# Optimization experiments

Measured on AMD Instinct MI355X. Metric: run time of the kernel, lower is better.

## Reference

```python
import jax, jax.numpy as jnp
import numpy as np

D_MODEL = 1024
H = 16
D_H = D_MODEL // H


def setup_inputs() -> dict:
    key = jax.random.key(0)
    ks = jax.random.split(key, 10)
    B, T_dec, T_enc = 2, 2048, 2048
    s = 1.0 / np.sqrt(D_MODEL)
    return {
        "tgt": jax.random.normal(ks[0], (B, T_dec, D_MODEL), jnp.float32),
        "memory": jax.random.normal(ks[1], (B, T_enc, D_MODEL), jnp.float32),
        "W_q": jax.random.normal(ks[2], (D_MODEL, D_MODEL), jnp.float32) * s,
        "b_q": jnp.zeros((D_MODEL,), jnp.float32),
        "W_k": jax.random.normal(ks[3], (D_MODEL, D_MODEL), jnp.float32) * s,
        "b_k": jnp.zeros((D_MODEL,), jnp.float32),
        "W_v": jax.random.normal(ks[4], (D_MODEL, D_MODEL), jnp.float32) * s,
        "b_v": jnp.zeros((D_MODEL,), jnp.float32),
        "W_o": jax.random.normal(ks[5], (D_MODEL, D_MODEL), jnp.float32) * s,
        "b_o": jnp.zeros((D_MODEL,), jnp.float32),
    }


def reference(tgt, memory, W_q, b_q, W_k, b_k, W_v, b_v, W_o, b_o):
    B, T_dec, _ = tgt.shape
    T_enc = memory.shape[1]
    # Projections (nn.Linear: x @ W^T + b; here W stored as (in,out) so x @ W + b)
    Q = tgt @ W_q + b_q          # (B, T_dec, d_model)
    K = memory @ W_k + b_k       # (B, T_enc, d_model)
    V = memory @ W_v + b_v       # (B, T_enc, d_model)
    # split heads: (B, h, T, d_h)
    Q = Q.reshape(B, T_dec, H, D_H).transpose(0, 2, 1, 3)
    K = K.reshape(B, T_enc, H, D_H).transpose(0, 2, 1, 3)
    V = V.reshape(B, T_enc, H, D_H).transpose(0, 2, 1, 3)
    # scores (B, h, T_dec, T_enc)
    S = jnp.einsum("bhqd,bhkd->bhqk", Q, K) / jnp.sqrt(jnp.float32(D_H)).astype(Q.dtype)
    A = jax.nn.softmax(S, axis=-1)
    Y = jnp.einsum("bhqk,bhkd->bhqd", A, V)
    Y = Y.transpose(0, 2, 1, 3).reshape(B, T_dec, D_MODEL)
    return Y @ W_o + b_o
```

## Files before the change

kernel.cpp:

```cpp
#include <hip/hip_runtime.h>
#include <hip/hip_bf16.h>
#include <stdint.h>

typedef unsigned short u16;
typedef __attribute__((ext_vector_type(8))) short bf16x8;
typedef __attribute__((ext_vector_type(4))) short bf16x4;
typedef __attribute__((ext_vector_type(4))) float f32x4;

__device__ __forceinline__ float bf2f(u16 u) {
    union { unsigned int i; float f; } v; v.i = ((unsigned int)u) << 16; return v.f;
}
__device__ __forceinline__ u16 f2bf(float f) {
    union { float f; unsigned int i; } v; v.f = f;
    unsigned int x = v.i;
    return (u16)((x + 0x7fffu + ((x >> 16) & 1u)) >> 16);
}
__device__ __forceinline__ unsigned fbits(float f) {
    union { float f; unsigned int i; } v; v.f = f; return v.i;
}
__device__ __forceinline__ void async16(const void* g, void* lds) {
    __builtin_amdgcn_global_load_lds((const __attribute__((address_space(1))) void*)g,
                                     (__attribute__((address_space(3))) void*)lds,
                                     16, 0, 0);
}

#define QSCALE 0.18033688f

__global__ __launch_bounds__(256) void prep(
    const float* __restrict__ tgt, const float* __restrict__ mem,
    const float* __restrict__ Wq, const float* __restrict__ Wk,
    const float* __restrict__ Wv, const float* __restrict__ Wo,
    u16* __restrict__ Wt, u16* __restrict__ tgtb, u16* __restrict__ memb)
{
    __shared__ u16 tile[64][65];
    const int id = blockIdx.x;
    const int tid = threadIdx.x;
    if (id < 1024) {
        const int z = id >> 8;
        const float* in = (z == 0) ? Wq : (z == 1) ? Wk : (z == 2) ? Wv : Wo;
        u16* out = Wt + (size_t)z * 1048576;
        const int k0 = (id & 15) * 64, n0 = ((id >> 4) & 15) * 64;
        const int r = tid >> 2, c0 = (tid & 3) << 4;
#pragma unroll
        for (int i = 0; i < 4; ++i) {
            float4 v = *(const float4*)&in[(size_t)(k0 + r) * 1024 + n0 + c0 + i * 4];
            tile[c0 + i * 4 + 0][r] = f2bf(v.x);
            tile[c0 + i * 4 + 1][r] = f2bf(v.y);
            tile[c0 + i * 4 + 2][r] = f2bf(v.z);
            tile[c0 + i * 4 + 3][r] = f2bf(v.w);
        }
        __syncthreads();
#pragma unroll
        for (int i = 0; i < 2; ++i) {
            bf16x8 v;
#pragma unroll
            for (int j = 0; j < 8; ++j) v[j] = (short)tile[r][c0 + i * 8 + j];
            *(bf16x8*)&out[(size_t)(n0 + r) * 1024 + k0 + c0 + i * 8] = v;
        }
    } else {
        size_t i = ((size_t)(id - 1024) * 256 + tid) * 8;
        float4 a0 = *(const float4*)&tgt[i];
        float4 a1 = *(const float4*)&tgt[i + 4];
        float4 b0 = *(const float4*)&mem[i];
        float4 b1 = *(const float4*)&mem[i + 4];
        bf16x8 va, vb;
        va[0] = (short)f2bf(a0.x); va[1] = (short)f2bf(a0.y);
        va[2] = (short)f2bf(a0.z); va[3] = (short)f2bf(a0.w);
        va[4] = (short)f2bf(a1.x); va[5] = (short)f2bf(a1.y);
        va[6] = (short)f2bf(a1.z); va[7] = (short)f2bf(a1.w);
        vb[0] = (short)f2bf(b0.x); vb[1] = (short)f2bf(b0.y);
        vb[2] = (short)f2bf(b0.z); vb[3] = (short)f2bf(b0.w);
        vb[4] = (short)f2bf(b1.x); vb[5] = (short)f2bf(b1.y);
        vb[6] = (short)f2bf(b1.z); vb[7] = (short)f2bf(b1.w);
        *(bf16x8*)&tgtb[i] = va;
        *(bf16x8*)&memb[i] = vb;
    }
}

__global__ __launch_bounds__(256) void gemm_qkv(
    const u16* __restrict__ tgtb, const u16* __restrict__ memb,
    const u16* __restrict__ Wt,
    const float* __restrict__ bq, const float* __restrict__ bk, const float* __restrict__ bv,
    u16* __restrict__ Qb, u16* __restrict__ Kb, u16* __restrict__ Vtb)
{
    __shared__ __align__(16) u16 sA[2][128 * 32];
    __shared__ __align__(16) u16 sB[2][128 * 32];
    const int z = blockIdx.z;
    const u16* A = (z == 0) ? tgtb : memb;
    const u16* Bt = Wt + (size_t)z * 1048576;
    const float* bias = (z == 0) ? bq : (z == 1) ? bk : bv;

    const int tid = threadIdx.x;
    const int wave = tid >> 6, lane = tid & 63;
    const int quad = lane >> 4, l16 = lane & 15;
    const int m0 = blockIdx.x * 128, n0 = blockIdx.y * 128;
    const int wm = (wave & 1) * 64, wn = (wave >> 1) * 64;
    const int sw = (quad ^ ((l16 >> 1) & 3)) << 3;

    f32x4 acc[4][4] = {};

#define GSTAGE(k0, buf)                                                       \
    {                                                                         \
        _Pragma("unroll")                                                     \
        for (int r = 0; r < 2; ++r) {                                         \
            int c = tid + r * 256;                                            \
            int g = (c & 3) ^ ((c >> 3) & 3);                                 \
            const u16* gA = A + (size_t)(m0 + (c >> 2)) * 1024 + (k0) + g * 8;\
            async16(gA, (char*)&sA[buf][0] + r * 4096 + wave * 1024);         \
            const u16* gB = Bt + (size_t)(n0 + (c >> 2)) * 1024 + (k0) + g * 8;\
            async16(gB, (char*)&sB[buf][0] + r * 4096 + wave * 1024);         \
        }                                                                     \
    }

    GSTAGE(0, 0);

    for (int it = 0; it < 32; ++it) {
        __syncthreads();
        if (it < 31) GSTAGE((it + 1) * 32, (it + 1) & 1);
        const u16* a = &sA[it & 1][0];
        const u16* bb_ = &sB[it & 1][0];
        bf16x8 af[4], bfr[4];
#pragma unroll
        for (int i = 0; i < 4; ++i) {
            af[i]  = *(const bf16x8*)&a[(wm + i * 16 + l16) * 32 + sw];
            bfr[i] = *(const bf16x8*)&bb_[(wn + i * 16 + l16) * 32 + sw];
        }
#pragma unroll
        for (int i = 0; i < 4; ++i)
#pragma unroll
            for (int j = 0; j < 4; ++j)
                acc[i][j] = __builtin_amdgcn_mfma_f32_16x16x32_bf16(af[i], bfr[j], acc[i][j], 0, 0, 0);
    }
#undef GSTAGE

    if (z == 2) {
#pragma unroll
        for (int j = 0; j < 4; ++j) {
            int n = n0 + wn + j * 16 + l16;
            float bb = bias[n];
            int d = n & 63;
#pragma unroll
            for (int i = 0; i < 4; ++i) {
                int mb = m0 + wm + i * 16 + quad * 4;
                int bh = (mb >> 11) * 16 + (n >> 6);
                bf16x4 pk;
#pragma unroll
                for (int r = 0; r < 4; ++r) pk[r] = (short)f2bf(acc[i][j][r] + bb);
                *(bf16x4*)&Vtb[(size_t)bh * 131072 + (size_t)d * 2048 + (mb & 2047)] = pk;
            }
        }
    } else {
        u16* C = (z == 0) ? Qb : Kb;
        const float scl = (z == 0) ? QSCALE : 1.0f;
#pragma unroll
        for (int j = 0; j < 4; ++j) {
            int n = n0 + wn + j * 16 + l16;
            float bb = bias[n];
#pragma unroll
            for (int i = 0; i < 4; ++i) {
                int mb = m0 + wm + i * 16 + quad * 4;
#pragma unroll
                for (int r = 0; r < 4; ++r)
                    C[(size_t)(mb + r) * 1024 + n] = f2bf((acc[i][j][r] + bb) * scl);
            }
        }
    }
}

__global__ __launch_bounds__(256) void gemm_out(
    const u16* __restrict__ A, const u16* __restrict__ Bt,
    const float* __restrict__ bias, float* __restrict__ C)
{
    __shared__ __align__(16) u16 sA[2][64 * 32];
    __shared__ __align__(16) u16 sB[2][128 * 32];
    const int tid = threadIdx.x;
    const int wave = tid >> 6, lane = tid & 63;
    const int quad = lane >> 4, l16 = lane & 15;
    const int m0 = blockIdx.x * 64, n0 = blockIdx.y * 128;
    const int wm = (wave & 1) * 32, wn = (wave >> 1) * 64;
    const int sw = (quad ^ ((l16 >> 1) & 3)) << 3;
    f32x4 acc[2][4] = {};

#define OSTAGE(k0, buf)                                                       \
    {                                                                         \
        {                                                                     \
            int c = tid;                                                      \
            int g = (c & 3) ^ ((c >> 3) & 3);                                 \
            const u16* gA = A + (size_t)(m0 + (c >> 2)) * 1024 + (k0) + g * 8;\
            async16(gA, (char*)&sA[buf][0] + wave * 1024);                    \
        }                                                                     \
        _Pragma("unroll")                                                     \
        for (int r = 0; r < 2; ++r) {                                         \
            int c = tid + r * 256;                                            \
            int g = (c & 3) ^ ((c >> 3) & 3);                                 \
            const u16* gB = Bt + (size_t)(n0 + (c >> 2)) * 1024 + (k0) + g * 8;\
            async16(gB, (char*)&sB[buf][0] + r * 4096 + wave * 1024);         \
        }                                                                     \
    }

    OSTAGE(0, 0);

    for (int it = 0; it < 32; ++it) {
        __syncthreads();
        if (it < 31) OSTAGE((it + 1) * 32, (it + 1) & 1);
        const u16* a = &sA[it & 1][0];
        const u16* bb_ = &sB[it & 1][0];
        bf16x8 af[2], bfr[4];
#pragma unroll
        for (int i = 0; i < 2; ++i)
            af[i] = *(const bf16x8*)&a[(wm + i * 16 + l16) * 32 + sw];
#pragma unroll
        for (int j = 0; j < 4; ++j)
            bfr[j] = *(const bf16x8*)&bb_[(wn + j * 16 + l16) * 32 + sw];
#pragma unroll
        for (int i = 0; i < 2; ++i)
#pragma unroll
            for (int j = 0; j < 4; ++j)
                acc[i][j] = __builtin_amdgcn_mfma_f32_16x16x32_bf16(af[i], bfr[j], acc[i][j], 0, 0, 0);
    }
#undef OSTAGE

#pragma unroll
    for (int j = 0; j < 4; ++j) {
        int n = n0 + wn + j * 16 + l16;
        float bb = bias[n];
#pragma unroll
        for (int i = 0; i < 2; ++i) {
            int mb = m0 + wm + i * 16 + quad * 4;
#pragma unroll
            for (int r = 0; r < 4; ++r)
                C[(size_t)(mb + r) * 1024 + n] = acc[i][j][r] + bb;
        }
    }
}

__global__ __launch_bounds__(256, 2) void attn_kernel(
    const u16* __restrict__ Q,
    const u16* __restrict__ K,
    const u16* __restrict__ Vt,
    u16* __restrict__ Y)
{
    __shared__ __align__(16) u16 sK[2][4096];
    __shared__ __align__(16) u16 sV[2][4096];

    const int tid = threadIdx.x;
    const int wave = tid >> 6, lane = tid & 63;
    const int quad = lane >> 4, l16 = lane & 15;

    const int bidx = blockIdx.x;
    const int bh = (bidx & 7) * 4 + ((bidx >> 3) & 3);
    const int qt = bidx >> 5;
    const int b = bh >> 4, h = bh & 15;
    const size_t qrow0 = (size_t)b * 2048 + qt * 128;
    const int st = ((qt << 1) | (bh & 1)) & 31;

    const size_t qrowA = qrow0 + wave * 32 + l16;
    const size_t qrowB = qrowA + 16;
    bf16x8 qA0 = *(const bf16x8*)&Q[qrowA * 1024 + h * 64 + quad * 8];
    bf16x8 qA1 = *(const bf16x8*)&Q[qrowA * 1024 + h * 64 + 32 + quad * 8];
    bf16x8 qB0 = *(const bf16x8*)&Q[qrowB * 1024 + h * 64 + quad * 8];
    bf16x8 qB1 = *(const bf16x8*)&Q[qrowB * 1024 + h * 64 + 32 + quad * 8];

    f32x4 oA[4] = {}, oB[4] = {};
    float rowA = 0.0f, rowB = 0.0f;

    const u16* Kbase = K + (size_t)b * 2048 * 1024 + h * 64;
    const u16* Vbase = Vt + (size_t)bh * 131072;

    const int x7 = l16 & 7;
    int koff[2], voff[4];
#pragma unroll
    for (int kf = 0; kf < 2; ++kf)
        koff[kf] = (l16 * 8 + ((kf * 4 + quad) ^ x7)) * 8;
#pragma unroll
    for (int ks = 0; ks < 4; ++ks)
        voff[ks] = (l16 * 8 + ((ks * 2 + (quad >> 1)) ^ x7)) * 8 + (quad & 1) * 4;

#define STAGE1(kv0, buf, r)                                                   \
    {                                                                         \
        int c = tid + (r) * 256;                                              \
        int srow = c >> 3;                                                    \
        int g = (c & 7) ^ (srow & 7);                                         \
        async16(Kbase + (size_t)((kv0) + srow) * 1024 + g * 8,                \
                (char*)&sK[buf][0] + (r) * 4096 + wave * 1024);               \
        async16(Vbase + (size_t)srow * 2048 + (kv0) + g * 8,                  \
                (char*)&sV[buf][0] + (r) * 4096 + wave * 1024);               \
    }
#define STAGE(kv0, buf) STAGE1(kv0, buf, 0) STAGE1(kv0, buf, 1)

    STAGE(st * 64, 0);

    for (int i = 0; i < 32; ++i) {
        __syncthreads();
        if (i < 31) {
            int kvn = ((st + i + 1) & 31) * 64;
            STAGE(kvn, (i + 1) & 1);
        }
        const u16* kb = &sK[i & 1][0];
        const u16* vb = &sV[i & 1][0];

        bf16x8 kfr[4][2];
        bf16x4 vfr[4][4];
#pragma unroll
        for (int ks = 0; ks < 4; ++ks) {
            kfr[ks][0] = *(const bf16x8*)&kb[ks * 1024 + koff[0]];
            kfr[ks][1] = *(const bf16x8*)&kb[ks * 1024 + koff[1]];
        }
#pragma unroll
        for (int mt = 0; mt < 4; ++mt)
#pragma unroll
            for (int ks = 0; ks < 4; ++ks)
                vfr[mt][ks] = *(const bf16x4*)&vb[mt * 1024 + voff[ks]];

        __builtin_amdgcn_s_setprio(1);
#pragma unroll
        for (int ks = 0; ks < 4; ++ks) {
            f32x4 sA = {0.f, 0.f, 0.f, 0.f};
            f32x4 sB = {0.f, 0.f, 0.f, 0.f};
            sA = __builtin_amdgcn_mfma_f32_16x16x32_bf16(kfr[ks][0], qA0, sA, 0, 0, 0);
            sB = __builtin_amdgcn_mfma_f32_16x16x32_bf16(kfr[ks][0], qB0, sB, 0, 0, 0);
            sA = __builtin_amdgcn_mfma_f32_16x16x32_bf16(kfr[ks][1], qA1, sA, 0, 0, 0);
            sB = __builtin_amdgcn_mfma_f32_16x16x32_bf16(kfr[ks][1], qB1, sB, 0, 0, 0);
            float a0 = __builtin_amdgcn_exp2f(sA[0]);
            float a1 = __builtin_amdgcn_exp2f(sA[1]);
            float a2 = __builtin_amdgcn_exp2f(sA[2]);
            float a3 = __builtin_amdgcn_exp2f(sA[3]);
            float b0 = __builtin_amdgcn_exp2f(sB[0]);
            float b1 = __builtin_amdgcn_exp2f(sB[1]);
            float b2 = __builtin_amdgcn_exp2f(sB[2]);
            float b3 = __builtin_amdgcn_exp2f(sB[3]);
            rowA += (a0 + a1) + (a2 + a3);
            rowB += (b0 + b1) + (b2 + b3);
            unsigned loA = __builtin_amdgcn_perm(fbits(a1) + 0x8000u, fbits(a0) + 0x8000u, 0x07060302u);
            unsigned hiA = __builtin_amdgcn_perm(fbits(a3) + 0x8000u, fbits(a2) + 0x8000u, 0x07060302u);
            unsigned loB = __builtin_amdgcn_perm(fbits(b1) + 0x8000u, fbits(b0) + 0x8000u, 0x07060302u);
            unsigned hiB = __builtin_amdgcn_perm(fbits(b3) + 0x8000u, fbits(b2) + 0x8000u, 0x07060302u);
            union { unsigned u[2]; bf16x4 v; } pA, pB;
            pA.u[0] = loA; pA.u[1] = hiA;
            pB.u[0] = loB; pB.u[1] = hiB;
#pragma unroll
            for (int mt = 0; mt < 4; ++mt) {
                oA[mt] = __builtin_amdgcn_mfma_f32_16x16x16bf16_1k(vfr[mt][ks], pA.v, oA[mt], 0, 0, 0);
                oB[mt] = __builtin_amdgcn_mfma_f32_16x16x16bf16_1k(vfr[mt][ks], pB.v, oB[mt], 0, 0, 0);
            }
        }
        __builtin_amdgcn_s_setprio(0);
    }
#undef STAGE
#undef STAGE1

    rowA += __shfl_xor(rowA, 16, 64);
    rowA += __shfl_xor(rowA, 32, 64);
    rowB += __shfl_xor(rowB, 16, 64);
    rowB += __shfl_xor(rowB, 32, 64);
    const float invA = 1.0f / rowA;
    const float invB = 1.0f / rowB;

#pragma unroll
    for (int mt = 0; mt < 4; ++mt) {
        bf16x4 oa, ob;
#pragma unroll
        for (int r = 0; r < 4; ++r) {
            oa[r] = (short)f2bf(oA[mt][r] * invA);
            ob[r] = (short)f2bf(oB[mt][r] * invB);
        }
        *(bf16x4*)&Y[qrowA * 1024 + h * 64 + mt * 16 + quad * 4] = oa;
        *(bf16x4*)&Y[qrowB * 1024 + h * 64 + mt * 16 + quad * 4] = ob;
    }
}

extern "C" void kernel_launch(void* const* d_in, const int* in_sizes, int n_in,
                              void* d_out, int out_size, void* d_ws, size_t ws_size,
                              hipStream_t stream) {
    const float* tgt = (const float*)d_in[0];
    const float* mem = (const float*)d_in[1];
    const float* Wq  = (const float*)d_in[2];
    const float* bq  = (const float*)d_in[3];
    const float* Wk  = (const float*)d_in[4];
    const float* bk  = (const float*)d_in[5];
    const float* Wv  = (const float*)d_in[6];
    const float* bv  = (const float*)d_in[7];
    const float* Wo  = (const float*)d_in[8];
    const float* bo  = (const float*)d_in[9];

    u16* ws = (u16*)d_ws;
    const size_t SZ = 4194304;
    u16* Wt   = ws;
    u16* tgtb = ws + 4 * SZ;
    u16* memb = tgtb + SZ;
    u16* Qb   = memb + SZ;
    u16* Kb   = Qb + SZ;
    u16* Vtb  = Kb + SZ;
    u16* Yb   = Vtb + SZ;
    float* out = (float*)d_out;

    prep<<<dim3(3072), 256, 0, stream>>>(tgt, mem, Wq, Wk, Wv, Wo, Wt, tgtb, memb);
    gemm_qkv<<<dim3(32, 8, 3), 256, 0, stream>>>(tgtb, memb, Wt, bq, bk, bv, Qb, Kb, Vtb);
    attn_kernel<<<dim3(512), 256, 0, stream>>>(Qb, Kb, Vtb, Yb);
    gemm_out<<<dim3(64, 8), 256, 0, stream>>>(Yb, Wt + 3 * (size_t)1048576, bo, out);
}
```

Measured before the change: 220.3 us.

## Deepen GEMM prefetch to two stages with explicit vmcnt waits and barriers

The projection and output GEMM loops now issue the next two K-tiles up front. Each iteration waits only on the older outstanding async loads via s_waitcnt vmcnt instead of a full __syncthreads. A second barrier after the LDS fragment reads lets the buffer just consumed be refilled with tile it+2 while the MFMAs run, and those MFMAs get raised wave priority. The aim is to hide global-load latency behind compute. The hand-counted vmcnt values must match the exact number of loads per stage, and the extra barrier per iteration adds sync cost.

```diff
diff --git a/kernel.cpp b/kernel.cpp
--- a/kernel.cpp
+++ b/kernel.cpp
@@ -113,11 +113,16 @@
     }
 
     GSTAGE(0, 0);
+    GSTAGE(32, 1);
 
     for (int it = 0; it < 32; ++it) {
-        __syncthreads();
-        if (it < 31) GSTAGE((it + 1) * 32, (it + 1) & 1);
-        const u16* a = &sA[it & 1][0];
+        if (it < 31) { asm volatile("s_waitcnt vmcnt(4)" ::: "memory"); }
+        else         { asm volatile("s_waitcnt vmcnt(0)" ::: "memory"); }
+        __builtin_amdgcn_sched_barrier(0);
+        __builtin_amdgcn_s_barrier();
+        __builtin_amdgcn_sched_barrier(0);
+
+        const u16* a   = &sA[it & 1][0];
         const u16* bb_ = &sB[it & 1][0];
         bf16x8 af[4], bfr[4];
 #pragma unroll
@@ -125,11 +130,20 @@
             af[i]  = *(const bf16x8*)&a[(wm + i * 16 + l16) * 32 + sw];
             bfr[i] = *(const bf16x8*)&bb_[(wn + i * 16 + l16) * 32 + sw];
         }
+        asm volatile("s_waitcnt lgkmcnt(0)" ::: "memory");
+        __builtin_amdgcn_sched_barrier(0);
+        __builtin_amdgcn_s_barrier();
+        __builtin_amdgcn_sched_barrier(0);
+
+        if (it < 30) GSTAGE((it + 2) * 32, it & 1);
+
+        __builtin_amdgcn_s_setprio(1);
 #pragma unroll
         for (int i = 0; i < 4; ++i)
 #pragma unroll
             for (int j = 0; j < 4; ++j)
                 acc[i][j] = __builtin_amdgcn_mfma_f32_16x16x32_bf16(af[i], bfr[j], acc[i][j], 0, 0, 0);
+        __builtin_amdgcn_s_setprio(0);
     }
 #undef GSTAGE
 
@@ -199,11 +213,16 @@
     }
 
     OSTAGE(0, 0);
+    OSTAGE(32, 1);
 
     for (int it = 0; it < 32; ++it) {
-        __syncthreads();
-        if (it < 31) OSTAGE((it + 1) * 32, (it + 1) & 1);
-        const u16* a = &sA[it & 1][0];
+        if (it < 31) { asm volatile("s_waitcnt vmcnt(3)" ::: "memory"); }
+        else         { asm volatile("s_waitcnt vmcnt(0)" ::: "memory"); }
+        __builtin_amdgcn_sched_barrier(0);
+        __builtin_amdgcn_s_barrier();
+        __builtin_amdgcn_sched_barrier(0);
+
+        const u16* a   = &sA[it & 1][0];
         const u16* bb_ = &sB[it & 1][0];
         bf16x8 af[2], bfr[4];
 #pragma unroll
@@ -212,11 +231,20 @@
 #pragma unroll
         for (int j = 0; j < 4; ++j)
             bfr[j] = *(const bf16x8*)&bb_[(wn + j * 16 + l16) * 32 + sw];
+        asm volatile("s_waitcnt lgkmcnt(0)" ::: "memory");
+        __builtin_amdgcn_sched_barrier(0);
+        __builtin_amdgcn_s_barrier();
+        __builtin_amdgcn_sched_barrier(0);
+
+        if (it < 30) OSTAGE((it + 2) * 32, it & 1);
+
+        __builtin_amdgcn_s_setprio(1);
 #pragma unroll
         for (int i = 0; i < 2; ++i)
 #pragma unroll
             for (int j = 0; j < 4; ++j)
                 acc[i][j] = __builtin_amdgcn_mfma_f32_16x16x32_bf16(af[i], bfr[j], acc[i][j], 0, 0, 0);
+        __builtin_amdgcn_s_setprio(0);
     }
 #undef OSTAGE
 
```

Result: faster. 209.9 us (-4.7%).
